# Kernel tuning notes

Hardware: AMD Instinct MI355X
Metric: run time of the kernel (lower is better)

Reference implementation:

```python
import jax, jax.numpy as jnp
import numpy as np

N = 100000
D = 64
E = 1000000


def setup_inputs() -> dict:
    key = jax.random.key(0)
    k_x, k_e, k_w1, k_b1, k_w2, k_b2 = jax.random.split(key, 6)
    x = jax.random.normal(k_x, (N, D), dtype=jnp.float32)
    edge_index = jax.random.randint(k_e, (2, E), 0, N, dtype=jnp.int64)
    # nn.Linear(2D, D): weight [D, 2D], bias [D]
    lim1 = 1.0 / np.sqrt(2 * D)
    W1 = jax.random.uniform(k_w1, (D, 2 * D), dtype=jnp.float32, minval=-lim1, maxval=lim1)
    b1 = jax.random.uniform(k_b1, (D,), dtype=jnp.float32, minval=-lim1, maxval=lim1)
    # nn.Linear(D, 1): weight [1, D], bias [1]
    lim2 = 1.0 / np.sqrt(D)
    W2 = jax.random.uniform(k_w2, (1, D), dtype=jnp.float32, minval=-lim2, maxval=lim2)
    b2 = jax.random.uniform(k_b2, (1,), dtype=jnp.float32, minval=-lim2, maxval=lim2)
    return {"x": x, "edge_index": edge_index, "W1": W1, "b1": b1, "W2": W2, "b2": b2}


def reference(x, edge_index, W1, b1, W2, b2):
    src = edge_index[0]
    dst = edge_index[1]
    # [E, 2D] gathered edge features
    edge_features = jnp.concatenate([x[src], x[dst]], axis=1)
    h = jax.nn.relu(edge_features @ W1.T + b1)  # [E, D]
    out = h @ W2.T + b2                          # [E, 1]
    return out.squeeze(-1)                       # [E]
```

## Files before the change

### kernel.cpp

```cpp
#include <hip/hip_runtime.h>

#define NDIM 64
#define FDIM 128

typedef _Float16 half8 __attribute__((ext_vector_type(8)));
typedef float    float4v __attribute__((ext_vector_type(4)));

__global__ __launch_bounds__(256) void node_gemm_kernel(
    const float* __restrict__ x,
    const float* __restrict__ W1,
    const float* __restrict__ b1,
    _Float16* __restrict__ Yab,
    int N)
{
    const int wave = threadIdx.x >> 6;
    const int lane = threadIdx.x & 63;
    const int c = lane & 15;
    const int g = lane >> 4;

    const int node0 = (blockIdx.x * 4 + wave) * 16;
    if (node0 >= N) return;

    float4v C[8];
    #pragma unroll
    for (int nt = 0; nt < 8; nt++) C[nt] = (float4v){0.f, 0.f, 0.f, 0.f};

    #pragma unroll
    for (int kk = 0; kk < 2; kk++) {
        const float* ap = x + (size_t)(node0 + c) * NDIM + kk * 32 + g * 8;
        float4v a0 = *(const float4v*)ap;
        float4v a1 = *(const float4v*)(ap + 4);
        half8 A;
        A[0] = (_Float16)a0[0]; A[1] = (_Float16)a0[1];
        A[2] = (_Float16)a0[2]; A[3] = (_Float16)a0[3];
        A[4] = (_Float16)a1[0]; A[5] = (_Float16)a1[1];
        A[6] = (_Float16)a1[2]; A[7] = (_Float16)a1[3];

        #pragma unroll
        for (int nt = 0; nt < 8; nt++) {
            const int jj = nt * 16 + c;
            const float* bp = W1 + (size_t)(jj & 63) * FDIM + (jj >> 6) * 64
                              + kk * 32 + g * 8;
            float4v w0 = *(const float4v*)bp;
            float4v w1 = *(const float4v*)(bp + 4);
            half8 B;
            B[0] = (_Float16)w0[0]; B[1] = (_Float16)w0[1];
            B[2] = (_Float16)w0[2]; B[3] = (_Float16)w0[3];
            B[4] = (_Float16)w1[0]; B[5] = (_Float16)w1[1];
            B[6] = (_Float16)w1[2]; B[7] = (_Float16)w1[3];
            C[nt] = __builtin_amdgcn_mfma_f32_16x16x32_f16(A, B, C[nt], 0, 0, 0);
        }
    }

    #pragma unroll
    for (int nt = 0; nt < 8; nt++) {
        const float badd = (nt < 4) ? b1[nt * 16 + c] : 0.f;
        #pragma unroll
        for (int r = 0; r < 4; r++) {
            Yab[(size_t)(node0 + g * 4 + r) * FDIM + nt * 16 + c] =
                (_Float16)(C[nt][r] + badd);
        }
    }
}

__global__ __launch_bounds__(256) void edge_combine_kernel(
    const _Float16* __restrict__ Yab,
    const int* __restrict__ ei,
    const float* __restrict__ W2,
    const float* __restrict__ b2,
    float* __restrict__ out,
    int E)
{
    int e = blockIdx.x * blockDim.x + threadIdx.x;
    if (e >= E) return;
    int s = ei[e];
    int d = ei[E + e];
    const half8* pa = (const half8*)(Yab + (size_t)s * FDIM);
    const half8* pb = (const half8*)(Yab + (size_t)d * FDIM + 64);

    half8 a[8], b[8];
    #pragma unroll
    for (int i = 0; i < 8; i++) { a[i] = pa[i]; b[i] = pb[i]; }

    float acc = 0.f;
    #pragma unroll
    for (int i = 0; i < 8; i++) {
        #pragma unroll
        for (int u = 0; u < 8; u++) {
            float h = (float)a[i][u] + (float)b[i][u];
            h = h > 0.f ? h : 0.f;
            acc = fmaf(W2[i * 8 + u], h, acc);
        }
    }
    out[e] = acc + b2[0];
}

__global__ __launch_bounds__(256) void edge_mlp_fp32_kernel(
    const float* __restrict__ x, const int* __restrict__ ei,
    const float* __restrict__ W1, const float* __restrict__ b1,
    const float* __restrict__ W2, const float* __restrict__ b2,
    float* __restrict__ out, int E)
{
    int e = blockIdx.x * blockDim.x + threadIdx.x;
    if (e >= E) return;
    int s = ei[e];
    int d = ei[E + e];
    const float* xs = x + (size_t)s * NDIM;
    const float* xd = x + (size_t)d * NDIM;
    float acc = b2[0];
    for (int j = 0; j < NDIM; j++) {
        float h = b1[j];
        for (int k = 0; k < NDIM; k++) {
            h += xs[k] * W1[j * FDIM + k] + xd[k] * W1[j * FDIM + 64 + k];
        }
        acc += W2[j] * (h > 0.f ? h : 0.f);
    }
    out[e] = acc;
}

extern "C" void kernel_launch(void* const* d_in, const int* in_sizes, int n_in,
                              void* d_out, int out_size, void* d_ws, size_t ws_size,
                              hipStream_t stream) {
    const float* x  = (const float*)d_in[0];
    const int*   ei = (const int*)d_in[1];
    const float* W1 = (const float*)d_in[2];
    const float* b1 = (const float*)d_in[3];
    const float* W2 = (const float*)d_in[4];
    const float* b2 = (const float*)d_in[5];
    float* out = (float*)d_out;
    const int E = out_size;
    const int N = in_sizes[0] / NDIM;

    const size_t tbl_bytes = (size_t)N * FDIM * sizeof(_Float16);

    if (ws_size >= tbl_bytes && (N % 16) == 0) {
        _Float16* Yab = (_Float16*)d_ws;
        const int nblocks = (N + 63) / 64;
        node_gemm_kernel<<<nblocks, 256, 0, stream>>>(x, W1, b1, Yab, N);
        edge_combine_kernel<<<(E + 255) / 256, 256, 0, stream>>>(
            Yab, ei, W2, b2, out, E);
    } else {
        edge_mlp_fp32_kernel<<<(E + 255) / 256, 256, 0, stream>>>(
            x, ei, W1, b1, W2, b2, out, E);
    }
}
```

Baseline: 162.0 us.

## Cooperatively gather edge rows with 8 lanes per edge and shuffle-reduce

The edge combine kernel now assigns 8 lanes to each edge, so each lane loads one 16-byte chunk of the source and destination rows. Each row is therefore read as contiguous coalesced segments instead of one thread issuing 16 strided vector loads. Partial dot products are reduced with xor shuffles, and each lane keeps one edge's result for a coalesced store. This adds a requirement that E be a multiple of 64, and it repeats the index loads across the 8 lanes of a group.

```diff
diff --git a/kernel.cpp b/kernel.cpp
--- a/kernel.cpp
+++ b/kernel.cpp
@@ -71,28 +71,40 @@
     float* __restrict__ out,
     int E)
 {
-    int e = blockIdx.x * blockDim.x + threadIdx.x;
-    if (e >= E) return;
-    int s = ei[e];
-    int d = ei[E + e];
-    const half8* pa = (const half8*)(Yab + (size_t)s * FDIM);
-    const half8* pb = (const half8*)(Yab + (size_t)d * FDIM + 64);
+    const int lane = threadIdx.x & 63;
+    const int wave = threadIdx.x >> 6;
+    const int grp  = lane >> 3;
+    const int j8   = lane & 7;
 
-    half8 a[8], b[8];
+    const long e0 = (long)blockIdx.x * 256 + wave * 64;
+    if (e0 >= E) return;
+
+    float4v w2lo = *(const float4v*)(W2 + j8 * 8);
+    float4v w2hi = *(const float4v*)(W2 + j8 * 8 + 4);
+    const float b2v = b2[0];
+
+    float keep = 0.f;
     #pragma unroll
-    for (int i = 0; i < 8; i++) { a[i] = pa[i]; b[i] = pb[i]; }
+    for (int t = 0; t < 8; t++) {
+        const long e = e0 + t * 8 + grp;
+        const int s = ei[e];
+        const int d = ei[E + e];
+        half8 a = *(const half8*)(Yab + (size_t)s * FDIM + j8 * 8);
+        half8 b = *(const half8*)(Yab + (size_t)d * FDIM + 64 + j8 * 8);
 
-    float acc = 0.f;
-    #pragma unroll
-    for (int i = 0; i < 8; i++) {
+        float acc = 0.f;
         #pragma unroll
         for (int u = 0; u < 8; u++) {
-            float h = (float)a[i][u] + (float)b[i][u];
+            float h = (float)a[u] + (float)b[u];
             h = h > 0.f ? h : 0.f;
-            acc = fmaf(W2[i * 8 + u], h, acc);
+            acc = fmaf(u < 4 ? w2lo[u] : w2hi[u - 4], h, acc);
         }
+        acc += __shfl_xor(acc, 1, 64);
+        acc += __shfl_xor(acc, 2, 64);
+        acc += __shfl_xor(acc, 4, 64);
+        if (j8 == t) keep = acc;
     }
-    out[e] = acc + b2[0];
+    out[e0 + j8 * 8 + grp] = keep + b2v;
 }
 
 __global__ __launch_bounds__(256) void edge_mlp_fp32_kernel(
@@ -133,7 +145,7 @@
 
     const size_t tbl_bytes = (size_t)N * FDIM * sizeof(_Float16);
 
-    if (ws_size >= tbl_bytes && (N % 16) == 0) {
+    if (ws_size >= tbl_bytes && (N % 16) == 0 && (E % 64) == 0) {
         _Float16* Yab = (_Float16*)d_ws;
         const int nblocks = (N + 63) / 64;
         node_gemm_kernel<<<nblocks, 256, 0, stream>>>(x, W1, b1, Yab, N);
```

Result: faster. 143.9 us (-11.2%).
